# Performance work log

Hardware: AMD Instinct MI355X
Metric: run time of the kernel (lower is better)

## Reference

```python
import jax, jax.numpy as jnp
import numpy as np

KH, KW = 3, 3
STRIDE = 1
OUT_C = 512


def im2col(x, kh, kw, stride):
    # x: [N, C, H, W] -> col: [C*kh*kw, N*oh*ow]  (row order: C major, then kh, kw)
    N, C, H, W = x.shape
    oh = (H - kh) // stride + 1
    ow = (W - kw) // stride + 1
    rows = jnp.arange(oh)[:, None] * stride + jnp.arange(kh)[None, :]  # [oh, kh]
    cols = jnp.arange(ow)[:, None] * stride + jnp.arange(kw)[None, :]  # [ow, kw]
    # gather windows: result [N, C, oh, kh, ow, kw]
    A = x[:, :, rows[:, :, None, None], cols[None, None, :, :]]
    # permute to (C, kh, kw, N, oh, ow) then flatten, matching torch permute(1,4,5,0,2,3)
    col = jnp.transpose(A, (1, 3, 5, 0, 2, 4)).reshape(C * kh * kw, N * oh * ow)
    return col, oh, ow


def setup_inputs() -> dict:
    key = jax.random.key(0)
    k1, k2, k3 = jax.random.split(key, 3)
    N, C, H, W = 16, 256, 32, 32
    K_sel = (C * KH * KW) // 2  # 1152 rows kept by the binary mask
    x = jax.random.normal(k1, (N, C, H, W), dtype=jnp.float32)
    weight = jax.random.normal(k2, (K_sel, OUT_C), dtype=jnp.float32) * 0.02
    idx = jnp.sort(jax.random.randint(k3, (K_sel,), 0, C * KH * KW, dtype=jnp.int32))
    return {"x": x, "weight": weight, "idx": idx}


def reference(x, weight, idx):
    N = x.shape[0]
    col, oh, ow = im2col(x, KH, KW, STRIDE)          # [C*kh*kw, N*oh*ow]
    x_tile = col[idx, :].T                            # gather masked rows -> [N*oh*ow, K_sel]
    conv_out = x_tile @ weight                        # [N*oh*ow, out_c]
    conv_out = conv_out.reshape(N, oh * ow, OUT_C)
    conv_out = jnp.transpose(conv_out, (0, 2, 1)).reshape(N, OUT_C, oh, ow)
    return conv_out
```

## Files before the change

kernel.cpp:

```cpp
#include <hip/hip_runtime.h>
#include <stdint.h>

#define N_IMG   16
#define C_IN    256
#define H_IN    32
#define W_IN    32
#define OH      30
#define OW      30
#define K_SEL   1152
#define OUTC    512
#define RY_TOT  (N_IMG * OH)
#define M_HAT   (RY_TOT * 32)
#define X_ELEMS (N_IMG * C_IN * H_IN * W_IN)
#define OUT_SP  (OH * OW)
#define CHW     (C_IN * H_IN * W_IN)

#define TO      128
#define TM      64
#define NMT     (M_HAT / TM)
#define NOT     (OUTC / TO)
#define BSTR    40
#define KITER   (K_SEL / 32)

typedef float f32x4  __attribute__((ext_vector_type(4)));
typedef short bf16x8 __attribute__((ext_vector_type(8)));

__device__ __forceinline__ unsigned short f2bf(float f) {
    unsigned int u = __float_as_uint(f);
    u += 0x7FFFu + ((u >> 16) & 1u);
    return (unsigned short)(u >> 16);
}

__device__ __forceinline__ void gl_lds16(const void* g, void* lds) {
    __builtin_amdgcn_global_load_lds(
        (const __attribute__((address_space(1))) unsigned int*)g,
        (__attribute__((address_space(3))) unsigned int*)lds,
        16, 0, 0);
}

__global__ void prep_kernel(const int* __restrict__ idx, const float* __restrict__ w,
                            int* __restrict__ koff, unsigned short* __restrict__ wT) {
    __shared__ float tile[32][33];
    const int bx = blockIdx.x, by = blockIdx.y, t = threadIdx.x;

    if (by == 0) {
        int k = bx * 256 + t;
        if (k < K_SEL) {
            int v = idx[k];
            int c = v / 9, rem = v - c * 9;
            int i = rem / 3, j = rem - i * 3;
            koff[k] = c * (H_IN * W_IN) + i * W_IN + j;
        }
    }
    const int s0 = bx * 32, o0 = by * 32;
    const int oc = t & 31, sg = t >> 5;
#pragma unroll
    for (int i = 0; i < 4; ++i) {
        int sl = sg * 4 + i;
        tile[sl][oc] = w[(s0 + sl) * OUTC + o0 + oc];
    }
    __syncthreads();
    const int ol = t >> 3, sq = t & 7;
    unsigned int u0 = (unsigned int)f2bf(tile[sq * 4 + 0][ol]) |
                      ((unsigned int)f2bf(tile[sq * 4 + 1][ol]) << 16);
    unsigned int u1 = (unsigned int)f2bf(tile[sq * 4 + 2][ol]) |
                      ((unsigned int)f2bf(tile[sq * 4 + 3][ol]) << 16);
    uint2 pk; pk.x = u0; pk.y = u1;
    *reinterpret_cast<uint2*>(&wT[(size_t)(o0 + ol) * K_SEL + s0 + sq * 4]) = pk;
}

__global__ __launch_bounds__(256, 4)
void gemm_kernel(const unsigned short* __restrict__ wT, const float* __restrict__ x,
                 const int* __restrict__ koff, float* __restrict__ out) {
    __shared__ __align__(16) unsigned short As[2][TO * 32];
    __shared__ __align__(16) unsigned short Bs[2][TM * BSTR];
    __shared__ int koS[K_SEL];

    const int t    = threadIdx.x;
    const int wave = t >> 6;
    const int lane = t & 63;
    const int quad = lane >> 4;
    const int lo   = lane & 15;

    const int bid = blockIdx.x;
    const int mt  = bid % NMT;
    const int ot  = bid / NMT;
    const int oBase = ot * TO;
    const int mBase = mt * TM;

    for (int i = t; i < K_SEL; i += 256) koS[i] = koff[i];

    const int xw  = t & 31;
    int basex[2];
#pragma unroll
    for (int ry = 0; ry < 2; ++ry) {
        int ryg = mt * 2 + ry;
        int n = ryg / 30, y = ryg - n * 30;
        basex[ry] = n * CHW + y * W_IN + xw;
    }

    const int kq4 = t >> 5;
    const int ks  = kq4 * 4;

    const int lrow = lane >> 2, csw = (lane & 3) ^ ((lrow >> 1) & 3);
    const unsigned short* wrow0 = wT + (size_t)(oBase + wave * 32 + lrow) * K_SEL + csw * 8;
    const unsigned short* wrow1 = wT + (size_t)(oBase + wave * 32 + 16 + lrow) * K_SEL + csw * 8;
    unsigned short* lA0 = &As[0][(wave * 32) * 32];
    unsigned short* lA1 = &As[1][(wave * 32) * 32];

    const int aswz = quad ^ ((lo >> 1) & 3);
    const unsigned short* aB[2] = {
        &As[0][(wave * 32 + lo) * 32 + aswz * 8],
        &As[1][(wave * 32 + lo) * 32 + aswz * 8] };
    const unsigned short* bB[2] = {
        &Bs[0][lo * BSTR + quad * 8],
        &Bs[1][lo * BSTR + quad * 8] };
    unsigned short* bW[2] = {
        &Bs[0][xw * BSTR + ks],
        &Bs[1][xw * BSTR + ks] };

    __syncthreads();

    f32x4 acc[2][4] = {};
    float v[2][2][4];

    gl_lds16(wrow0, lA0);
    gl_lds16(wrow1, lA0 + 16 * 32);
    {
        int4 k4 = *(const int4*)&koS[ks];
#pragma unroll
        for (int ry = 0; ry < 2; ++ry)
#pragma unroll
            for (int j = 0; j < 4; ++j) {
                int g = basex[ry] + ((const int*)&k4)[j];
                g = min(g, X_ELEMS - 1);
                v[0][ry][j] = x[g];
            }
    }
#pragma unroll
    for (int ry = 0; ry < 2; ++ry) {
        unsigned int u0 = (unsigned int)f2bf(v[0][ry][0]) |
                          ((unsigned int)f2bf(v[0][ry][1]) << 16);
        unsigned int u1 = (unsigned int)f2bf(v[0][ry][2]) |
                          ((unsigned int)f2bf(v[0][ry][3]) << 16);
        uint2 pk; pk.x = u0; pk.y = u1;
        *reinterpret_cast<uint2*>(bW[0] + ry * 32 * BSTR) = pk;
    }
    {
        int4 k4 = *(const int4*)&koS[32 + ks];
#pragma unroll
        for (int ry = 0; ry < 2; ++ry)
#pragma unroll
            for (int j = 0; j < 4; ++j) {
                int g = basex[ry] + ((const int*)&k4)[j];
                g = min(g, X_ELEMS - 1);
                v[1][ry][j] = x[g];
            }
    }
    asm volatile("s_waitcnt lgkmcnt(0)" ::: "memory");
    __builtin_amdgcn_s_barrier();

#pragma unroll 2
    for (int kt = 0; kt < KITER; ++kt) {
        const int p = kt & 1, q = p ^ 1;
        unsigned short* lAq = q ? lA1 : lA0;

        {
            const int k1 = (kt + 1 < KITER ? kt + 1 : KITER - 1) * 32;
            gl_lds16(wrow0 + k1, lAq);
            gl_lds16(wrow1 + k1, lAq + 16 * 32);
        }
        {
            const int k2 = (kt + 2 < KITER ? kt + 2 : KITER - 1) * 32;
            int4 k4 = *(const int4*)&koS[k2 + ks];
#pragma unroll
            for (int ry = 0; ry < 2; ++ry)
#pragma unroll
                for (int j = 0; j < 4; ++j) {
                    int g = basex[ry] + ((const int*)&k4)[j];
                    g = min(g, X_ELEMS - 1);
                    v[p][ry][j] = x[g];
                }
        }
        asm volatile("s_waitcnt vmcnt(10)" ::: "memory");
#pragma unroll
        for (int ry = 0; ry < 2; ++ry) {
            unsigned int u0 = (unsigned int)f2bf(v[q][ry][0]) |
                              ((unsigned int)f2bf(v[q][ry][1]) << 16);
            unsigned int u1 = (unsigned int)f2bf(v[q][ry][2]) |
                              ((unsigned int)f2bf(v[q][ry][3]) << 16);
            uint2 pk; pk.x = u0; pk.y = u1;
            *reinterpret_cast<uint2*>(bW[q] + ry * 32 * BSTR) = pk;
        }
        bf16x8 a[2], b[4];
#pragma unroll
        for (int ms = 0; ms < 2; ++ms)
            a[ms] = *(const bf16x8*)(aB[p] + ms * 16 * 32);
#pragma unroll
        for (int ns = 0; ns < 4; ++ns)
            b[ns] = *(const bf16x8*)(bB[p] + ns * 16 * BSTR);
#pragma unroll
        for (int ms = 0; ms < 2; ++ms)
#pragma unroll
            for (int ns = 0; ns < 4; ++ns)
                acc[ms][ns] = __builtin_amdgcn_mfma_f32_16x16x32_bf16(
                    a[ms], b[ns], acc[ms][ns], 0, 0, 0);
        asm volatile("s_waitcnt lgkmcnt(0)" ::: "memory");
        __builtin_amdgcn_s_barrier();
    }

#pragma unroll
    for (int ns = 0; ns < 4; ++ns) {
        const int mh  = mBase + ns * 16 + lo;
        const int xwe = mh & 31;
        const int ryg = mh >> 5;
        const int n = ryg / 30, y = ryg - n * 30;
        if (xwe < OW) {
            const size_t ob = (size_t)n * (OUTC * OUT_SP) + (size_t)y * OW + xwe;
#pragma unroll
            for (int ms = 0; ms < 2; ++ms) {
                const int o0 = oBase + wave * 32 + ms * 16 + quad * 4;
#pragma unroll
                for (int r = 0; r < 4; ++r)
                    out[ob + (size_t)(o0 + r) * OUT_SP] = acc[ms][ns][r];
            }
        }
    }
}

extern "C" void kernel_launch(void* const* d_in, const int* in_sizes, int n_in,
                              void* d_out, int out_size, void* d_ws, size_t ws_size,
                              hipStream_t stream) {
    const float* x   = (const float*)d_in[0];
    const float* w   = (const float*)d_in[1];
    const int*   idx = (const int*)d_in[2];
    float*       out = (float*)d_out;

    char* ws = (char*)d_ws;
    int*            koff = (int*)ws;
    unsigned short* wT   = (unsigned short*)(ws + 4608);

    prep_kernel<<<dim3(K_SEL / 32, OUTC / 32), dim3(256), 0, stream>>>(idx, w, koff, wT);
    gemm_kernel<<<dim3(NMT * NOT), dim3(256), 0, stream>>>(wT, x, koff, out);
}
```

Before: 113.2 us.

## Double output-channel tile to 256 per block and clamp x column instead of index

Result: no change. 114.3 us (+1.0%).

```diff
diff --git a/kernel.cpp b/kernel.cpp
--- a/kernel.cpp
+++ b/kernel.cpp
@@ -15,7 +15,7 @@
 #define OUT_SP  (OH * OW)
 #define CHW     (C_IN * H_IN * W_IN)
 
-#define TO      128
+#define TO      256
 #define TM      64
 #define NMT     (M_HAT / TM)
 #define NOT     (OUTC / TO)
@@ -69,7 +69,7 @@
     *reinterpret_cast<uint2*>(&wT[(size_t)(o0 + ol) * K_SEL + s0 + sq * 4]) = pk;
 }
 
-__global__ __launch_bounds__(256, 4)
+__global__ __launch_bounds__(256, 2)
 void gemm_kernel(const unsigned short* __restrict__ wT, const float* __restrict__ x,
                  const int* __restrict__ koff, float* __restrict__ out) {
     __shared__ __align__(16) unsigned short As[2][TO * 32];
@@ -91,27 +91,34 @@
     for (int i = t; i < K_SEL; i += 256) koS[i] = koff[i];
 
     const int xw  = t & 31;
+    const int xwc = min(xw, 29);
     int basex[2];
 #pragma unroll
     for (int ry = 0; ry < 2; ++ry) {
         int ryg = mt * 2 + ry;
         int n = ryg / 30, y = ryg - n * 30;
-        basex[ry] = n * CHW + y * W_IN + xw;
+        basex[ry] = n * CHW + y * W_IN + xwc;
     }
 
     const int kq4 = t >> 5;
     const int ks  = kq4 * 4;
 
     const int lrow = lane >> 2, csw = (lane & 3) ^ ((lrow >> 1) & 3);
-    const unsigned short* wrow0 = wT + (size_t)(oBase + wave * 32 + lrow) * K_SEL + csw * 8;
-    const unsigned short* wrow1 = wT + (size_t)(oBase + wave * 32 + 16 + lrow) * K_SEL + csw * 8;
-    unsigned short* lA0 = &As[0][(wave * 32) * 32];
-    unsigned short* lA1 = &As[1][(wave * 32) * 32];
+    const unsigned short* wrow[4];
+#pragma unroll
+    for (int i = 0; i < 4; ++i)
+        wrow[i] = wT + (size_t)(oBase + wave * 64 + i * 16 + lrow) * K_SEL + csw * 8;
+    unsigned short* lA[2][4];
+#pragma unroll
+    for (int b = 0; b < 2; ++b)
+#pragma unroll
+        for (int i = 0; i < 4; ++i)
+            lA[b][i] = &As[b][(wave * 64 + i * 16) * 32];
 
     const int aswz = quad ^ ((lo >> 1) & 3);
     const unsigned short* aB[2] = {
-        &As[0][(wave * 32 + lo) * 32 + aswz * 8],
-        &As[1][(wave * 32 + lo) * 32 + aswz * 8] };
+        &As[0][(wave * 64 + lo) * 32 + aswz * 8],
+        &As[1][(wave * 64 + lo) * 32 + aswz * 8] };
     const unsigned short* bB[2] = {
         &Bs[0][lo * BSTR + quad * 8],
         &Bs[1][lo * BSTR + quad * 8] };
@@ -121,22 +128,18 @@
 
     __syncthreads();
 
-    f32x4 acc[2][4] = {};
+    f32x4 acc[4][4] = {};
     float v[2][2][4];
 
-    gl_lds16(wrow0, lA0);
-    gl_lds16(wrow1, lA0 + 16 * 32);
     {
         int4 k4 = *(const int4*)&koS[ks];
 #pragma unroll
         for (int ry = 0; ry < 2; ++ry)
 #pragma unroll
-            for (int j = 0; j < 4; ++j) {
-                int g = basex[ry] + ((const int*)&k4)[j];
-                g = min(g, X_ELEMS - 1);
-                v[0][ry][j] = x[g];
-            }
-    }
+            for (int j = 0; j < 4; ++j)
+                v[0][ry][j] = x[basex[ry] + ((const int*)&k4)[j]];
+    }
+    asm volatile("s_waitcnt vmcnt(0)" ::: "memory");
 #pragma unroll
     for (int ry = 0; ry < 2; ++ry) {
         unsigned int u0 = (unsigned int)f2bf(v[0][ry][0]) |
@@ -146,16 +149,15 @@
         uint2 pk; pk.x = u0; pk.y = u1;
         *reinterpret_cast<uint2*>(bW[0] + ry * 32 * BSTR) = pk;
     }
+#pragma unroll
+    for (int i = 0; i < 4; ++i) gl_lds16(wrow[i], lA[0][i]);
     {
         int4 k4 = *(const int4*)&koS[32 + ks];
 #pragma unroll
         for (int ry = 0; ry < 2; ++ry)
 #pragma unroll
-            for (int j = 0; j < 4; ++j) {
-                int g = basex[ry] + ((const int*)&k4)[j];
-                g = min(g, X_ELEMS - 1);
-                v[1][ry][j] = x[g];
-            }
+            for (int j = 0; j < 4; ++j)
+                v[1][ry][j] = x[basex[ry] + ((const int*)&k4)[j]];
     }
     asm volatile("s_waitcnt lgkmcnt(0)" ::: "memory");
     __builtin_amdgcn_s_barrier();
@@ -163,12 +165,11 @@
 #pragma unroll 2
     for (int kt = 0; kt < KITER; ++kt) {
         const int p = kt & 1, q = p ^ 1;
-        unsigned short* lAq = q ? lA1 : lA0;
 
         {
             const int k1 = (kt + 1 < KITER ? kt + 1 : KITER - 1) * 32;
-            gl_lds16(wrow0 + k1, lAq);
-            gl_lds16(wrow1 + k1, lAq + 16 * 32);
+#pragma unroll
+            for (int i = 0; i < 4; ++i) gl_lds16(wrow[i] + k1, lA[q][i]);
         }
         {
             const int k2 = (kt + 2 < KITER ? kt + 2 : KITER - 1) * 32;
@@ -176,13 +177,10 @@
 #pragma unroll
             for (int ry = 0; ry < 2; ++ry)
 #pragma unroll
-                for (int j = 0; j < 4; ++j) {
-                    int g = basex[ry] + ((const int*)&k4)[j];
-                    g = min(g, X_ELEMS - 1);
-                    v[p][ry][j] = x[g];
-                }
-        }
-        asm volatile("s_waitcnt vmcnt(10)" ::: "memory");
+                for (int j = 0; j < 4; ++j)
+                    v[p][ry][j] = x[basex[ry] + ((const int*)&k4)[j]];
+        }
+        asm volatile("s_waitcnt vmcnt(12)" ::: "memory");
 #pragma unroll
         for (int ry = 0; ry < 2; ++ry) {
             unsigned int u0 = (unsigned int)f2bf(v[q][ry][0]) |
@@ -192,15 +190,15 @@
             uint2 pk; pk.x = u0; pk.y = u1;
             *reinterpret_cast<uint2*>(bW[q] + ry * 32 * BSTR) = pk;
         }
-        bf16x8 a[2], b[4];
-#pragma unroll
-        for (int ms = 0; ms < 2; ++ms)
+        bf16x8 a[4], b[4];
+#pragma unroll
+        for (int ms = 0; ms < 4; ++ms)
             a[ms] = *(const bf16x8*)(aB[p] + ms * 16 * 32);
 #pragma unroll
         for (int ns = 0; ns < 4; ++ns)
             b[ns] = *(const bf16x8*)(bB[p] + ns * 16 * BSTR);
 #pragma unroll
-        for (int ms = 0; ms < 2; ++ms)
+        for (int ms = 0; ms < 4; ++ms)
 #pragma unroll
             for (int ns = 0; ns < 4; ++ns)
                 acc[ms][ns] = __builtin_amdgcn_mfma_f32_16x16x32_bf16(
@@ -218,8 +216,8 @@
         if (xwe < OW) {
             const size_t ob = (size_t)n * (OUTC * OUT_SP) + (size_t)y * OW + xwe;
 #pragma unroll
-            for (int ms = 0; ms < 2; ++ms) {
-                const int o0 = oBase + wave * 32 + ms * 16 + quad * 4;
+            for (int ms = 0; ms < 4; ++ms) {
+                const int o0 = oBase + wave * 64 + ms * 16 + quad * 4;
 #pragma unroll
                 for (int r = 0; r < 4; ++r)
                     out[ob + (size_t)(o0 + r) * OUT_SP] = acc[ms][ns][r];
```
